# Optimization experiments

Hardware: AMD Instinct MI355X
Metric: run time of the kernel (lower is better)

The kernel has to match this reference:

```python
import jax, jax.numpy as jnp
import numpy as np

HEAD_SIZE = 64
N_EMBD = 1024

def setup_inputs() -> dict:
    key = jax.random.key(0)
    ks = jax.random.split(key, 7)
    B, T = 4, 4096
    s = 1.0 / np.sqrt(N_EMBD)
    return {
        "x": jax.random.normal(ks[0], (B, T, N_EMBD), dtype=jnp.float32),
        "Wq": jax.random.normal(ks[1], (N_EMBD, HEAD_SIZE), dtype=jnp.float32) * s,
        "bq": jnp.zeros((HEAD_SIZE,), dtype=jnp.float32),
        "Wk": jax.random.normal(ks[2], (N_EMBD, HEAD_SIZE), dtype=jnp.float32) * s,
        "bk": jnp.zeros((HEAD_SIZE,), dtype=jnp.float32),
        "Wv": jax.random.normal(ks[3], (N_EMBD, HEAD_SIZE), dtype=jnp.float32) * s,
        "bv": jnp.zeros((HEAD_SIZE,), dtype=jnp.float32),
    }

def reference(x, Wq, bq, Wk, bk, Wv, bv):
    # q,k,v: [B,T,H]
    q = x @ Wq + bq
    k = x @ Wk + bk
    v = x @ Wv + bv
    scale = jnp.asarray(HEAD_SIZE, x.dtype) ** -0.5
    att = jnp.einsum("bth,bsh->bts", q, k) * scale  # [B,T,T]
    att = jax.nn.softmax(att, axis=-1)
    # dropout with p=0.0 is identity (eval-mode reference)
    return jnp.einsum("bts,bsh->bth", att, v)
```

## Files before the change

### kernel.cpp

```cpp
#include <hip/hip_runtime.h>
#include <hip/hip_bf16.h>
#include <cmath>

#define BATCH 4
#define TLEN  4096
#define CEMB  1024
#define HEAD  64
#define NROWS (BATCH * TLEN)

typedef __bf16 bf16;
typedef __attribute__((ext_vector_type(8))) __bf16 bf16x8;
typedef __attribute__((ext_vector_type(4))) __bf16 bf16x4;
typedef __attribute__((ext_vector_type(4))) float f32x4;
typedef __attribute__((ext_vector_type(16))) float f32x16;
typedef __attribute__((ext_vector_type(4))) unsigned u32x4;

#define QSCALE 0.1803368801111204f

static __device__ __forceinline__ f32x4 mfma16(bf16x8 a, bf16x8 b, f32x4 c) {
    return __builtin_amdgcn_mfma_f32_16x16x32_bf16(a, b, c, 0, 0, 0);
}
static __device__ __forceinline__ f32x16 mfma32(bf16x8 a, bf16x8 b, f32x16 c) {
    return __builtin_amdgcn_mfma_f32_32x32x16_bf16(a, b, c, 0, 0, 0);
}
static __device__ __forceinline__ unsigned cvt_pk_bf16(float lo, float hi) {
    unsigned r;
    asm("v_cvt_pk_bf16_f32 %0, %1, %2" : "=v"(r) : "v"(lo), "v"(hi));
    return r;
}

static __device__ __forceinline__ void async_ld16(const void* g, void* l) {
    __builtin_amdgcn_global_load_lds(
        (const __attribute__((address_space(1))) void*)g,
        (__attribute__((address_space(3))) void*)l, 16, 0, 0);
}

__global__ __launch_bounds__(256) void pack_w(
    const float* __restrict__ Wq, const float* __restrict__ Wk,
    const float* __restrict__ Wv, bf16* __restrict__ Wt)
{
    __shared__ float Wl[128][68];
    const int which = blockIdx.x >> 3;
    const int kb    = blockIdx.x & 7;
    const int t     = threadIdx.x;
    const float* W = which == 0 ? Wq : (which == 1 ? Wk : Wv);
    const float s = which == 0 ? QSCALE : 1.0f;

    const float4* Wf = (const float4*)(W + (size_t)kb * 128 * 64);
    #pragma unroll
    for (int i = 0; i < 8; ++i) {
        const int f = i * 256 + t;
        float4 w = Wf[f];
        *(float4*)&Wl[f >> 4][(f & 15) * 4] = w;
    }
    __syncthreads();

    const int lanex = t & 63;
    const int grp   = t >> 6;
    const int quad  = lanex >> 4, colx = lanex & 15;
    #pragma unroll
    for (int it = 0; it < 4; ++it) {
        const int seg = it * 4 + grp;
        const int jg4 = seg >> 2, h4 = seg & 3;
        bf16x8 o;
        #pragma unroll
        for (int e = 0; e < 8; ++e)
            o[e] = (bf16)(Wl[h4 * 32 + quad * 8 + e][jg4 * 16 + colx] * s);
        const int jg = which * 4 + jg4;
        const int h  = kb * 4 + h4;
        *(bf16x8*)(Wt + ((size_t)(jg * 32 + h) * 64 + lanex) * 8) = o;
    }
}

__global__ __launch_bounds__(256, 4) void qkv(
    const float* __restrict__ x, const bf16* __restrict__ Wt,
    const float* __restrict__ bq, const float* __restrict__ bk,
    const float* __restrict__ bv,
    bf16* __restrict__ qb, bf16* __restrict__ kb, bf16* __restrict__ vT)
{
    __shared__ __align__(16) float Xsh[2][2][16][64];

    const int tid  = threadIdx.x;
    const int lane = tid & 63;
    const int wvid = tid >> 6;
    const int quad = lane >> 4;
    const int col  = lane & 15;
    const int row0 = blockIdx.x * 16;

    const float* xblk = x + (size_t)row0 * CEMB;
    const bf16* wbase[3];
    #pragma unroll
    for (int j = 0; j < 3; ++j)
        wbase[j] = Wt + (size_t)(wvid * 3 + j) * 32 * 64 * 8 + (size_t)lane * 8;

    const int sr = lane >> 4;
    const int ss = lane & 15;
    auto stage = [&](int ci, int bufi) {
        #pragma unroll
        for (int h2 = 0; h2 < 2; ++h2) {
            const int r = wvid * 4 + sr;
            const int c = ss ^ (r & 7);
            async_ld16(xblk + (size_t)r * CEMB + ci * 128 + h2 * 64 + c * 4,
                       &Xsh[bufi][h2][wvid * 4][0]);
        }
    };

    f32x4 acc[3] = {};
    const int c7 = col & 7;

    stage(0, 0);
    int buf = 0;
    for (int ci = 0; ci < 8; ++ci) {
        __syncthreads();
        if (ci + 1 < 8) stage(ci + 1, buf ^ 1);

        #pragma unroll
        for (int kk = 0; kk < 4; ++kk) {
            const int h  = ci * 4 + kk;
            const int hf = kk >> 1;
            const int kl = kk & 1;
            bf16x8 Bv[3];
            #pragma unroll
            for (int j = 0; j < 3; ++j)
                Bv[j] = *(const bf16x8*)(wbase[j] + (size_t)h * 512);
            const int g0 = kl * 8 + quad * 2;
            float4 a0 = *(const float4*)&Xsh[buf][hf][col][(g0 ^ c7) * 4];
            float4 a1 = *(const float4*)&Xsh[buf][hf][col][((g0 + 1) ^ c7) * 4];
            bf16x8 af;
            af[0]=(bf16)a0.x; af[1]=(bf16)a0.y; af[2]=(bf16)a0.z; af[3]=(bf16)a0.w;
            af[4]=(bf16)a1.x; af[5]=(bf16)a1.y; af[6]=(bf16)a1.z; af[7]=(bf16)a1.w;
            #pragma unroll
            for (int j = 0; j < 3; ++j)
                acc[j] = mfma16(af, Bv[j], acc[j]);
        }
        buf ^= 1;
    }

    const float* bias[3] = {bq, bk, bv};
    #pragma unroll
    for (int j = 0; j < 3; ++j) {
        const int jg = wvid * 3 + j;
        const int which = jg >> 2;
        const int h = (jg & 3) * 16 + col;
        float bb = bias[which][h];
        if (which == 0) bb *= QSCALE;
        if (which < 2) {
            bf16* dst = which == 0 ? qb : kb;
            #pragma unroll
            for (int r = 0; r < 4; ++r) {
                const int trow = row0 + quad * 4 + r;
                dst[(size_t)trow * HEAD + h] = (bf16)(acc[j][r] + bb);
            }
        } else {
            bf16x4 pv;
            #pragma unroll
            for (int r = 0; r < 4; ++r) pv[r] = (bf16)(acc[j][r] + bb);
            const int trow0 = row0 + quad * 4;
            const int bb_   = trow0 >> 12;
            const int tt    = trow0 & (TLEN - 1);
            *(bf16x4*)(vT + ((size_t)(bb_ * HEAD + h)) * TLEN + tt) = pv;
        }
    }
}

__global__ __launch_bounds__(256, 2) void attn(
    const bf16* __restrict__ qb, const bf16* __restrict__ kb,
    const bf16* __restrict__ vT,
    bf16* __restrict__ opart, float* __restrict__ lpart,
    float* __restrict__ out, int nsplit, int lg2S)
{
    __shared__ __align__(16) bf16 Ksh[2][64][64];
    __shared__ __align__(16) bf16 Vsh[2][64][64];

    const int tid  = threadIdx.x;
    const int lane = tid & 63;
    const int wvid = tid >> 6;
    const int l31  = lane & 31;
    const int b5   = lane >> 5;

    int b, sp, qtile;
    {
        const int id = blockIdx.x;
        if (nsplit >= 2) {
            const int cpx = (BATCH << lg2S) >> 3;
            const int idx = id >> 3;
            const int combo = (id & 7) * cpx + (idx >> 4);
            qtile = idx & 15;
            b = combo >> lg2S;
            sp = combo & (nsplit - 1);
        } else {
            qtile = id & 15; b = id >> 4; sp = 0;
        }
    }
    const int q0 = qtile * 256 + wvid * 64;
    const size_t rowbase = (size_t)b * TLEN + q0;

    bf16x8 qf[2][4];
    #pragma unroll
    for (int qt = 0; qt < 2; ++qt)
        #pragma unroll
        for (int m = 0; m < 4; ++m)
            qf[qt][m] = *(const bf16x8*)
                (qb + (rowbase + qt * 32 + l31) * HEAD + m * 16 + b5 * 8);

    const bf16* kbB = kb + (size_t)b * TLEN * HEAD;
    const bf16* vTB = vT + (size_t)b * HEAD * TLEN;

    f32x16 o[2][2] = {};
    float lsum[2] = {0.f, 0.f};

    const int slen = TLEN >> lg2S;
    const int sbeg = sp * slen;
    const int nch  = slen / 64;

    const int r8 = lane >> 3;
    const int s8 = lane & 7;
    auto stage = [&](int s0, int bufi) {
        #pragma unroll
        for (int j = 0; j < 2; ++j) {
            const int r = wvid * 16 + j * 8 + r8;
            const int c = s8 ^ (r & 7);
            async_ld16(kbB + (size_t)(s0 + r) * HEAD + c * 8,
                       &Ksh[bufi][wvid * 16 + j * 8][0]);
            async_ld16(vTB + (size_t)r * TLEN + s0 + c * 8,
                       &Vsh[bufi][wvid * 16 + j * 8][0]);
        }
    };

    stage(sbeg, 0);
    int buf = 0;
    for (int ci = 0; ci < nch; ++ci) {
        __syncthreads();
        if (ci + 1 < nch) stage(sbeg + (ci + 1) * 64, buf ^ 1);

        #pragma unroll
        for (int kt = 0; kt < 2; ++kt) {
            const int kr = kt * 32 + l31;
            const int k7 = kr & 7;
            bf16x8 kf[4];
            #pragma unroll
            for (int m = 0; m < 4; ++m)
                kf[m] = *(const bf16x8*)&Ksh[buf][kr][((2 * m + b5) ^ k7) * 8];

            bf16x8 pb[2][2];
            #pragma unroll
            for (int qt = 0; qt < 2; ++qt) {
                f32x16 st = {};
                #pragma unroll
                for (int m = 0; m < 4; ++m)
                    st = mfma32(kf[m], qf[qt][m], st);
                float e[16];
                #pragma unroll
                for (int r = 0; r < 16; ++r)
                    e[r] = __builtin_amdgcn_exp2f(st[r]);
                float t0 = (e[0] + e[1]) + (e[2] + e[3]);
                float t1 = (e[4] + e[5]) + (e[6] + e[7]);
                float t2 = (e[8] + e[9]) + (e[10] + e[11]);
                float t3 = (e[12] + e[13]) + (e[14] + e[15]);
                lsum[qt] += (t0 + t1) + (t2 + t3);
                unsigned w[8];
                #pragma unroll
                for (int s = 0; s < 8; ++s)
                    w[s] = cvt_pk_bf16(e[2 * s], e[2 * s + 1]);
                #pragma unroll
                for (int kc = 0; kc < 2; ++kc) {
                    auto s02 = __builtin_amdgcn_permlane32_swap(
                        w[4 * kc + 0], w[4 * kc + 2], false, false);
                    auto s13 = __builtin_amdgcn_permlane32_swap(
                        w[4 * kc + 1], w[4 * kc + 3], false, false);
                    u32x4 pw = { (unsigned)s02[0], (unsigned)s13[0],
                                 (unsigned)s02[1], (unsigned)s13[1] };
                    pb[qt][kc] = __builtin_bit_cast(bf16x8, pw);
                }
            }
            #pragma unroll
            for (int ht = 0; ht < 2; ++ht) {
                const int vr = ht * 32 + l31;
                const int v7 = vr & 7;
                #pragma unroll
                for (int kc = 0; kc < 2; ++kc) {
                    bf16x8 vf = *(const bf16x8*)
                        &Vsh[buf][vr][((2 * (2 * kt + kc) + b5) ^ v7) * 8];
                    #pragma unroll
                    for (int qt = 0; qt < 2; ++qt)
                        o[qt][ht] = mfma32(vf, pb[qt][kc], o[qt][ht]);
                }
            }
        }
        buf ^= 1;
    }

    #pragma unroll
    for (int qt = 0; qt < 2; ++qt)
        lsum[qt] += __shfl_xor(lsum[qt], 32, 64);

    #pragma unroll
    for (int qt = 0; qt < 2; ++qt) {
        const size_t grow = rowbase + qt * 32 + l31;
        if (nsplit == 1) {
            const float inv = 1.f / lsum[qt];
            float* ob = out + grow * HEAD;
            #pragma unroll
            for (int ht = 0; ht < 2; ++ht)
                #pragma unroll
                for (int g = 0; g < 4; ++g) {
                    f32x4 r = { o[qt][ht][4*g+0] * inv, o[qt][ht][4*g+1] * inv,
                                o[qt][ht][4*g+2] * inv, o[qt][ht][4*g+3] * inv };
                    *(f32x4*)(ob + ht * 32 + g * 8 + b5 * 4) = r;
                }
        } else if (sp == 0) {
            float* ob = out + grow * HEAD;
            #pragma unroll
            for (int ht = 0; ht < 2; ++ht)
                #pragma unroll
                for (int g = 0; g < 4; ++g) {
                    f32x4 r = { o[qt][ht][4*g+0], o[qt][ht][4*g+1],
                                o[qt][ht][4*g+2], o[qt][ht][4*g+3] };
                    *(f32x4*)(ob + ht * 32 + g * 8 + b5 * 4) = r;
                }
            if (lane < 32) lpart[grow] = lsum[qt];
        } else {
            bf16* ob = opart + ((size_t)(sp - 1) * NROWS + grow) * HEAD;
            #pragma unroll
            for (int ht = 0; ht < 2; ++ht)
                #pragma unroll
                for (int g = 0; g < 4; ++g) {
                    bf16x4 r = { (bf16)o[qt][ht][4*g+0], (bf16)o[qt][ht][4*g+1],
                                 (bf16)o[qt][ht][4*g+2], (bf16)o[qt][ht][4*g+3] };
                    *(bf16x4*)(ob + ht * 32 + g * 8 + b5 * 4) = r;
                }
            if (lane < 32) lpart[(size_t)sp * NROWS + grow] = lsum[qt];
        }
    }
}

__global__ __launch_bounds__(256) void combine(
    const bf16* __restrict__ opart, const float* __restrict__ lpart,
    float* __restrict__ out, int nsplit)
{
    const int gid = blockIdx.x * 256 + threadIdx.x;
    const int row = gid >> 4;
    const int h4  = (gid & 15) * 4;

    float L = 0.f;
    for (int s = 0; s < nsplit; ++s) L += lpart[(size_t)s * NROWS + row];
    f32x4 O = *(const f32x4*)(out + (size_t)row * HEAD + h4);
    for (int s = 1; s < nsplit; ++s) {
        bf16x4 v = *(const bf16x4*)(opart + ((size_t)(s - 1) * NROWS + row) * HEAD + h4);
        O[0] += (float)v[0]; O[1] += (float)v[1];
        O[2] += (float)v[2]; O[3] += (float)v[3];
    }
    f32x4 r = O * (1.f / L);
    *(f32x4*)(out + (size_t)row * HEAD + h4) = r;
}

extern "C" void kernel_launch(void* const* d_in, const int* in_sizes, int n_in,
                              void* d_out, int out_size, void* d_ws, size_t ws_size,
                              hipStream_t stream) {
    const float* x  = (const float*)d_in[0];
    const float* Wq = (const float*)d_in[1];
    const float* bq = (const float*)d_in[2];
    const float* Wk = (const float*)d_in[3];
    const float* bk = (const float*)d_in[4];
    const float* Wv = (const float*)d_in[5];
    const float* bv = (const float*)d_in[6];
    float* out = (float*)d_out;

    const size_t n_tok = (size_t)NROWS * HEAD;
    char* ws = (char*)d_ws;
    bf16* qb = (bf16*)ws;
    bf16* kb = qb + n_tok;
    bf16* vT = kb + n_tok;
    bf16* Wt = vT + n_tok;
    const size_t base = 3 * n_tok * sizeof(bf16) + 192 * CEMB * sizeof(bf16);

    auto need = [&](int S) {
        return base + (size_t)(S - 1) * n_tok * sizeof(bf16)
                    + (size_t)S * NROWS * sizeof(float);
    };
    int S = 1, lg2S = 0;
    if      (ws_size >= need(8)) { S = 8; lg2S = 3; }
    else if (ws_size >= need(4)) { S = 4; lg2S = 2; }
    else if (ws_size >= need(2)) { S = 2; lg2S = 1; }
    bf16*  opart = Wt + 192 * CEMB;
    float* lpart = (float*)(opart + (size_t)(S - 1) * n_tok);

    pack_w<<<dim3(24), dim3(256), 0, stream>>>(Wq, Wk, Wv, Wt);
    qkv<<<dim3(1024), dim3(256), 0, stream>>>(x, Wt, bq, bk, bv, qb, kb, vT);
    attn<<<dim3(16 * BATCH * S), dim3(256), 0, stream>>>(
        qb, kb, vT, opart, lpart, out, S, lg2S);
    if (S > 1)
        combine<<<dim3((NROWS * 16) / 256), dim3(256), 0, stream>>>(
            opart, lpart, out, S);
}
```

Before: 155.1 us.

## Deepen async LDS prefetch pipelines with explicit vmcnt waits and raw barriers

The QKV projection kernel moves from double-buffered to 4-buffer staging with three chunks in flight. The attention kernel moves to triple-buffered K/V tiles with two chunks in flight. __syncthreads is replaced by raw s_barrier plus a partial s_waitcnt vmcnt, so later global->LDS loads stay outstanding while the current tile is consumed. This aims to hide global load latency better, at the cost of more LDS per block (which may reduce occupancy in attn) and hand-counted wait values that must match the number of loads issued.

```diff
diff --git a/kernel.cpp b/kernel.cpp
--- a/kernel.cpp
+++ b/kernel.cpp
@@ -33,6 +33,17 @@
     __builtin_amdgcn_global_load_lds(
         (const __attribute__((address_space(1))) void*)g,
         (__attribute__((address_space(3))) void*)l, 16, 0, 0);
+}
+
+static __device__ __forceinline__ void barx() {
+    asm volatile("s_barrier" ::: "memory");
+}
+static __device__ __forceinline__ void wait_vm(int n) {
+    if      (n >= 8) asm volatile("s_waitcnt vmcnt(8)" ::: "memory");
+    else if (n >= 6) asm volatile("s_waitcnt vmcnt(6)" ::: "memory");
+    else if (n >= 4) asm volatile("s_waitcnt vmcnt(4)" ::: "memory");
+    else if (n >= 2) asm volatile("s_waitcnt vmcnt(2)" ::: "memory");
+    else             asm volatile("s_waitcnt vmcnt(0)" ::: "memory");
 }
 
 __global__ __launch_bounds__(256) void pack_w(
@@ -78,7 +89,7 @@
     const float* __restrict__ bv,
     bf16* __restrict__ qb, bf16* __restrict__ kb, bf16* __restrict__ vT)
 {
-    __shared__ __align__(16) float Xsh[2][2][16][64];
+    __shared__ __align__(16) float Xsh[4][2][16][64];
 
     const int tid  = threadIdx.x;
     const int lane = tid & 63;
@@ -108,11 +119,14 @@
     f32x4 acc[3] = {};
     const int c7 = col & 7;
 
-    stage(0, 0);
-    int buf = 0;
+    stage(0, 0); stage(1, 1); stage(2, 2);
+    #pragma unroll
     for (int ci = 0; ci < 8; ++ci) {
-        __syncthreads();
-        if (ci + 1 < 8) stage(ci + 1, buf ^ 1);
+        barx();
+        if (ci + 3 < 8) stage(ci + 3, (ci + 3) & 3);
+        wait_vm(2 * (ci <= 4 ? 3 : 7 - ci));
+        barx();
+        const int buf = ci & 3;
 
         #pragma unroll
         for (int kk = 0; kk < 4; ++kk) {
@@ -133,7 +147,6 @@
             for (int j = 0; j < 3; ++j)
                 acc[j] = mfma16(af, Bv[j], acc[j]);
         }
-        buf ^= 1;
     }
 
     const float* bias[3] = {bq, bk, bv};
@@ -169,8 +182,8 @@
     bf16* __restrict__ opart, float* __restrict__ lpart,
     float* __restrict__ out, int nsplit, int lg2S)
 {
-    __shared__ __align__(16) bf16 Ksh[2][64][64];
-    __shared__ __align__(16) bf16 Vsh[2][64][64];
+    __shared__ __align__(16) bf16 Ksh[3][64][64];
+    __shared__ __align__(16) bf16 Vsh[3][64][64];
 
     const int tid  = threadIdx.x;
     const int lane = tid & 63;
@@ -228,10 +241,16 @@
     };
 
     stage(sbeg, 0);
-    int buf = 0;
+    if (nch > 1) stage(sbeg + 64, 1);
+    int buf = 0, sbuf = 2;
     for (int ci = 0; ci < nch; ++ci) {
-        __syncthreads();
-        if (ci + 1 < nch) stage(sbeg + (ci + 1) * 64, buf ^ 1);
+        barx();
+        if (ci + 2 < nch) stage(sbeg + (ci + 2) * 64, sbuf);
+        {
+            int n = nch - 1 - ci; if (n > 2) n = 2;
+            wait_vm(4 * n);
+        }
+        barx();
 
         #pragma unroll
         for (int kt = 0; kt < 2; ++kt) {
@@ -287,7 +306,8 @@
                 }
             }
         }
-        buf ^= 1;
+        buf  = (buf  == 2) ? 0 : buf  + 1;
+        sbuf = (sbuf == 2) ? 0 : sbuf + 1;
     }
 
     #pragma unroll
```

Measured after the change: 151.8 us. 1.02x faster.
